# Kernel optimization log

Measured on AMD Instinct MI355X. Metric: run time of the kernel, lower is better.

## Reference

```python
import jax, jax.numpy as jnp
import numpy as np

N_NODES = 100000
IMPROVED_FILL = 2.0  # improved=True in GCNConv -> self-loop weight 2.0


def setup_inputs() -> dict:
    key = jax.random.key(0)
    k1, k2, k3 = jax.random.split(key, 3)
    x = jax.random.normal(k1, (N_NODES, 128), dtype=jnp.float32)
    edge_index = jax.random.randint(k2, (2, 640000), 0, N_NODES, dtype=jnp.int64)
    # Glorot-style init like PyG's GCNConv weight
    W = jax.random.normal(k3, (128, 128), dtype=jnp.float32) * (1.0 / np.sqrt(128))
    b = jnp.zeros((128,), dtype=jnp.float32)
    return {"x": x, "edge_index": edge_index, "W": W, "b": b}


def reference(x, edge_index, W, b):
    N = x.shape[0]
    E = edge_index.shape[1]
    # --- gcn_norm with improved self-loops (fill value 2.0) ---
    loop = jnp.arange(N, dtype=edge_index.dtype)
    row = jnp.concatenate([edge_index[0], loop])  # source nodes
    col = jnp.concatenate([edge_index[1], loop])  # target nodes
    ew = jnp.concatenate([jnp.ones((E,), x.dtype), jnp.full((N,), IMPROVED_FILL, x.dtype)])
    deg = jax.ops.segment_sum(ew, col, num_segments=N)
    dinv = jnp.where(deg > 0, jax.lax.rsqrt(deg), 0.0)
    norm = dinv[row] * ew * dinv[col]  # [E+N]
    # --- linear transform then normalized scatter-add aggregation ---
    xW = x @ W  # [N, out]
    msgs = norm[:, None] * xW[row]  # [E+N, out]
    out = jax.ops.segment_sum(msgs, col, num_segments=N)
    return out + b
```

## Files before the change

kernel.cpp:

```cpp
#include <hip/hip_runtime.h>

#define GCN_N 100000
#define GCN_E 640000
#define GCN_F 128
#define NPB  32
#define CAP  32
#define ZROW 100000

typedef __attribute__((ext_vector_type(8))) short bf16x8;
typedef __attribute__((ext_vector_type(4))) float f32x4;
typedef __attribute__((ext_vector_type(8))) unsigned short ushort8;

__device__ inline unsigned short f2bf(float f) {
    unsigned u = __float_as_uint(f);
    return (unsigned short)((u + 0x7fff + ((u >> 16) & 1)) >> 16);
}
__device__ inline float bflo(unsigned u) { return __uint_as_float(u << 16); }
__device__ inline float bfhi(unsigned u) { return __uint_as_float(u & 0xffff0000u); }

__global__ void fill_ell(const int* __restrict__ rows, const int* __restrict__ cols,
                         int* __restrict__ cnt, int* __restrict__ ell) {
    int i = blockIdx.x * 256 + threadIdx.x;
    int4 r = ((const int4*)rows)[i];
    int4 c = ((const int4*)cols)[i];
    int k;
    k = atomicAdd(&cnt[c.x], 1); if (k < CAP) ell[(size_t)c.x * CAP + k] = r.x;
    k = atomicAdd(&cnt[c.y], 1); if (k < CAP) ell[(size_t)c.y * CAP + k] = r.y;
    k = atomicAdd(&cnt[c.z], 1); if (k < CAP) ell[(size_t)c.z * CAP + k] = r.z;
    k = atomicAdd(&cnt[c.w], 1); if (k < CAP) ell[(size_t)c.w * CAP + k] = r.w;
}

__global__ void scale_conv(const float* __restrict__ x, const int* __restrict__ cnt,
                           ushort* __restrict__ xs, const float* __restrict__ W,
                           ushort* __restrict__ wfh, ushort* __restrict__ wfl) {
    int blk = blockIdx.x;
    int t = threadIdx.x;
    if (blk >= 12501) {
        int p    = blk - 12501;
        int pi   = p * 4 + (t >> 6);
        int lane = t & 63;
        int kt = pi >> 3, nt = pi & 7;
        int kr   = kt * 32 + ((lane >> 4) * 8);
        int ncol = nt * 16 + (lane & 15);
        ushort8 hv, lv;
#pragma unroll
        for (int j = 0; j < 8; ++j) {
            float w = W[(size_t)(kr + j) * GCN_F + ncol];
            unsigned short h = f2bf(w);
            hv[j] = h;
            lv[j] = f2bf(w - bflo((unsigned)h));
        }
        size_t fo = (size_t)(kt * 8 + nt) * 64 + lane;
        ((ushort8*)wfh)[fo] = hv;
        ((ushort8*)wfl)[fo] = lv;
        return;
    }
    if (blk == 12500) {
        if (t < 32) ((ushort4*)xs)[(size_t)ZROW * 32 + t] = make_ushort4(0, 0, 0, 0);
        return;
    }
    int i = blk * 256 + t;
    int node = i >> 5;
    float di = rsqrtf(2.0f + (float)cnt[node]);
    float4 v = ((const float4*)x)[i];
    ushort4 o;
    o.x = f2bf(di * v.x); o.y = f2bf(di * v.y);
    o.z = f2bf(di * v.z); o.w = f2bf(di * v.w);
    ((ushort4*)xs)[i] = o;
}

__global__ __launch_bounds__(256) void gcn_fused(
        const ushort* __restrict__ xs, const int* __restrict__ cnt,
        const int* __restrict__ ell, const ushort* __restrict__ wfh,
        const ushort* __restrict__ wfl, const float* __restrict__ b,
        float* __restrict__ out) {
    __shared__ ushort Ah[NPB * GCN_F];
    __shared__ ushort Al[NPB * GCN_F];
    __shared__ int    sell[NPB * CAP];
    __shared__ int    scnt[NPB];
    int t = threadIdx.x;
    int row0 = blockIdx.x * NPB;

    if (t < NPB) scnt[t] = cnt[row0 + t];
    __syncthreads();

    for (int i = t; i < NPB * CAP; i += 256) {
        int rr = i >> 5, kk = i & (CAP - 1);
        int v = ell[(size_t)(row0 + rr) * CAP + kk];
        int dg = scnt[rr]; if (dg > CAP) dg = CAP;
        sell[i] = (kk < dg) ? v : ZROW;
    }
    __syncthreads();

    int lane = t & 63;
    int wv   = t >> 6;

    {
        const unsigned* xs2 = (const unsigned*)xs;
        for (int q = 0; q < 8; ++q) {
            int rr = wv * 8 + q;
            int c  = row0 + rr;
            int deg = scnt[rr]; if (deg > CAP) deg = CAP;
            const int* sp = &sell[rr * CAP];
            int4 m0 = *(const int4*)sp;
            int4 m1 = *(const int4*)(sp + 4);
            unsigned sv = xs2[c * 64 + lane];
            unsigned v0 = xs2[m0.x * 64 + lane];
            unsigned v1 = xs2[m0.y * 64 + lane];
            unsigned v2 = xs2[m0.z * 64 + lane];
            unsigned v3 = xs2[m0.w * 64 + lane];
            unsigned v4 = xs2[m1.x * 64 + lane];
            unsigned v5 = xs2[m1.y * 64 + lane];
            unsigned v6 = xs2[m1.z * 64 + lane];
            unsigned v7 = xs2[m1.w * 64 + lane];
            float ax = 2.0f * bflo(sv);
            float ay = 2.0f * bfhi(sv);
            ax += bflo(v0) + bflo(v1) + bflo(v2) + bflo(v3)
                + bflo(v4) + bflo(v5) + bflo(v6) + bflo(v7);
            ay += bfhi(v0) + bfhi(v1) + bfhi(v2) + bfhi(v3)
                + bfhi(v4) + bfhi(v5) + bfhi(v6) + bfhi(v7);
            if (deg > 8) {
                for (int k = 8; k < deg; k += 4) {
                    int4 m = *(const int4*)(sp + k);
                    unsigned u0 = xs2[m.x * 64 + lane];
                    unsigned u1 = xs2[m.y * 64 + lane];
                    unsigned u2 = xs2[m.z * 64 + lane];
                    unsigned u3 = xs2[m.w * 64 + lane];
                    ax += bflo(u0) + bflo(u1) + bflo(u2) + bflo(u3);
                    ay += bfhi(u0) + bfhi(u1) + bfhi(u2) + bfhi(u3);
                }
            }
            float di = rsqrtf(2.0f + (float)scnt[rr]);
            float axd = di * ax, ayd = di * ay;
            unsigned short hx = f2bf(axd), hy = f2bf(ayd);
            unsigned short lx = f2bf(axd - bflo((unsigned)hx));
            unsigned short ly = f2bf(ayd - bflo((unsigned)hy));
            unsigned off = (unsigned)rr * 256 + (((unsigned)lane * 4) ^ (((unsigned)(rr & 7)) << 4));
            *(unsigned*)((char*)Ah + off) = ((unsigned)hy << 16) | hx;
            *(unsigned*)((char*)Al + off) = ((unsigned)ly << 16) | lx;
        }
    }
    __syncthreads();

    int lrow  = lane & 15;
    int lhalf = lane >> 4;
    f32x4 acc[2][2];
#pragma unroll
    for (int m = 0; m < 2; ++m)
#pragma unroll
        for (int n = 0; n < 2; ++n) acc[m][n] = (f32x4)0.f;

    const bf16x8* whp = (const bf16x8*)wfh;
    const bf16x8* wlp = (const bf16x8*)wfl;
    int nt0 = wv * 2;

#pragma unroll
    for (int kt = 0; kt < 4; ++kt) {
        unsigned kb = ((unsigned)(kt * 64 + lhalf * 16)) ^ (((unsigned)(lane & 7)) << 4);
        unsigned o0 = (unsigned)lrow * 256 + kb;
        bf16x8 ah[2], al[2], wh[2], wl[2];
        ah[0] = *(const bf16x8*)((const char*)Ah + o0);
        ah[1] = *(const bf16x8*)((const char*)Ah + o0 + 4096);
        al[0] = *(const bf16x8*)((const char*)Al + o0);
        al[1] = *(const bf16x8*)((const char*)Al + o0 + 4096);
        wh[0] = whp[(kt * 8 + nt0) * 64 + lane];
        wh[1] = whp[(kt * 8 + nt0 + 1) * 64 + lane];
        wl[0] = wlp[(kt * 8 + nt0) * 64 + lane];
        wl[1] = wlp[(kt * 8 + nt0 + 1) * 64 + lane];
#pragma unroll
        for (int m = 0; m < 2; ++m)
#pragma unroll
            for (int n = 0; n < 2; ++n) {
                acc[m][n] = __builtin_amdgcn_mfma_f32_16x16x32_bf16(ah[m], wh[n], acc[m][n], 0, 0, 0);
                acc[m][n] = __builtin_amdgcn_mfma_f32_16x16x32_bf16(ah[m], wl[n], acc[m][n], 0, 0, 0);
                acc[m][n] = __builtin_amdgcn_mfma_f32_16x16x32_bf16(al[m], wh[n], acc[m][n], 0, 0, 0);
            }
    }

    float b0 = b[wv * 32 + lrow];
    float b1 = b[wv * 32 + 16 + lrow];
#pragma unroll
    for (int m = 0; m < 2; ++m)
#pragma unroll
        for (int n = 0; n < 2; ++n) {
            int col = wv * 32 + n * 16 + lrow;
            float bb = n ? b1 : b0;
#pragma unroll
            for (int j = 0; j < 4; ++j) {
                int r = row0 + m * 16 + lhalf * 4 + j;
                out[(size_t)r * GCN_F + col] = acc[m][n][j] + bb;
            }
        }
}

extern "C" void kernel_launch(void* const* d_in, const int* in_sizes, int n_in,
                              void* d_out, int out_size, void* d_ws, size_t ws_size,
                              hipStream_t stream) {
    const float* x  = (const float*)d_in[0];
    const int*   ei = (const int*)d_in[1];
    const float* W  = (const float*)d_in[2];
    const float* b  = (const float*)d_in[3];
    float* out = (float*)d_out;

    const int N = GCN_N, E = GCN_E;
    const int* rows = ei;
    const int* cols = ei + E;

    char*   ws  = (char*)d_ws;
    int*    cnt = (int*)(ws + 0);
    int*    ell = (int*)(ws + 400384);
    ushort* xs  = (ushort*)(ws + 13200384);
    ushort* wfh = (ushort*)(ws + 38800640);
    ushort* wfl = (ushort*)(ws + 38833408);

    hipMemsetAsync(cnt, 0, (size_t)N * sizeof(int), stream);
    fill_ell<<<E / 1024, 256, 0, stream>>>(rows, cols, cnt, ell);
    scale_conv<<<12509, 256, 0, stream>>>(x, cnt, xs, W, wfh, wfl);
    gcn_fused<<<N / NPB, 256, 0, stream>>>(xs, cnt, ell, wfh, wfl, b, out);
}
```

Before: 182.9 us.

## Merge all GCN stages into one persistent kernel with grid barriers

Replaces the memset and three separate launches with a single persistent kernel of 1024 blocks that runs zeroing, ELL fill, feature scaling and the fused aggregate+GEMM stage, separated by software grid barriers. The ELL array is now pre-filled with the zero-row index, so the per-tile padding logic goes away and the adjacency tile loads straight into shared memory. Launch overhead and inter-kernel gaps are removed. In exchange it adds a full 12.8MB ELL initialization write, atomic spin barriers, and relies on all 1024 blocks being co-resident. Edge processing also drops from 4 edges per thread with int4 loads to grid-stride scalar loads.

```diff
diff --git a/kernel.cpp b/kernel.cpp
--- a/kernel.cpp
+++ b/kernel.cpp
@@ -6,6 +6,8 @@
 #define NPB  32
 #define CAP  32
 #define ZROW 100000
+#define GRID 1024
+#define TTOT (GRID * 256)
 
 typedef __attribute__((ext_vector_type(8))) short bf16x8;
 typedef __attribute__((ext_vector_type(4))) float f32x4;
@@ -18,89 +20,106 @@
 __device__ inline float bflo(unsigned u) { return __uint_as_float(u << 16); }
 __device__ inline float bfhi(unsigned u) { return __uint_as_float(u & 0xffff0000u); }
 
-__global__ void fill_ell(const int* __restrict__ rows, const int* __restrict__ cols,
-                         int* __restrict__ cnt, int* __restrict__ ell) {
-    int i = blockIdx.x * 256 + threadIdx.x;
-    int4 r = ((const int4*)rows)[i];
-    int4 c = ((const int4*)cols)[i];
-    int k;
-    k = atomicAdd(&cnt[c.x], 1); if (k < CAP) ell[(size_t)c.x * CAP + k] = r.x;
-    k = atomicAdd(&cnt[c.y], 1); if (k < CAP) ell[(size_t)c.y * CAP + k] = r.y;
-    k = atomicAdd(&cnt[c.z], 1); if (k < CAP) ell[(size_t)c.z * CAP + k] = r.z;
-    k = atomicAdd(&cnt[c.w], 1); if (k < CAP) ell[(size_t)c.w * CAP + k] = r.w;
-}
-
-__global__ void scale_conv(const float* __restrict__ x, const int* __restrict__ cnt,
-                           ushort* __restrict__ xs, const float* __restrict__ W,
-                           ushort* __restrict__ wfh, ushort* __restrict__ wfl) {
-    int blk = blockIdx.x;
-    int t = threadIdx.x;
-    if (blk >= 12501) {
-        int p    = blk - 12501;
-        int pi   = p * 4 + (t >> 6);
-        int lane = t & 63;
-        int kt = pi >> 3, nt = pi & 7;
-        int kr   = kt * 32 + ((lane >> 4) * 8);
-        int ncol = nt * 16 + (lane & 15);
-        ushort8 hv, lv;
-#pragma unroll
-        for (int j = 0; j < 8; ++j) {
-            float w = W[(size_t)(kr + j) * GCN_F + ncol];
-            unsigned short h = f2bf(w);
-            hv[j] = h;
-            lv[j] = f2bf(w - bflo((unsigned)h));
-        }
-        size_t fo = (size_t)(kt * 8 + nt) * 64 + lane;
-        ((ushort8*)wfh)[fo] = hv;
-        ((ushort8*)wfl)[fo] = lv;
-        return;
-    }
-    if (blk == 12500) {
-        if (t < 32) ((ushort4*)xs)[(size_t)ZROW * 32 + t] = make_ushort4(0, 0, 0, 0);
-        return;
-    }
-    int i = blk * 256 + t;
-    int node = i >> 5;
-    float di = rsqrtf(2.0f + (float)cnt[node]);
-    float4 v = ((const float4*)x)[i];
-    ushort4 o;
-    o.x = f2bf(di * v.x); o.y = f2bf(di * v.y);
-    o.z = f2bf(di * v.z); o.w = f2bf(di * v.w);
-    ((ushort4*)xs)[i] = o;
-}
-
-__global__ __launch_bounds__(256) void gcn_fused(
-        const ushort* __restrict__ xs, const int* __restrict__ cnt,
-        const int* __restrict__ ell, const ushort* __restrict__ wfh,
-        const ushort* __restrict__ wfl, const float* __restrict__ b,
-        float* __restrict__ out) {
+__device__ inline void grid_barrier(int* bar) {
+    __syncthreads();
+    if (threadIdx.x == 0) {
+        __threadfence();
+        int g = __hip_atomic_load(&bar[1], __ATOMIC_RELAXED, __HIP_MEMORY_SCOPE_AGENT);
+        int a = __hip_atomic_fetch_add(&bar[0], 1, __ATOMIC_ACQ_REL, __HIP_MEMORY_SCOPE_AGENT);
+        if (a == GRID - 1) {
+            __hip_atomic_store(&bar[0], 0, __ATOMIC_RELAXED, __HIP_MEMORY_SCOPE_AGENT);
+            __hip_atomic_fetch_add(&bar[1], 1, __ATOMIC_RELEASE, __HIP_MEMORY_SCOPE_AGENT);
+        } else {
+            while (__hip_atomic_load(&bar[1], __ATOMIC_ACQUIRE, __HIP_MEMORY_SCOPE_AGENT) == g) {
+                __builtin_amdgcn_s_sleep(2);
+            }
+        }
+        __threadfence();
+    }
+    __syncthreads();
+}
+
+__global__ __launch_bounds__(256, 4) void gcn_all(
+        const float* __restrict__ x, const int* __restrict__ rows,
+        const int* __restrict__ cols, const float* __restrict__ W,
+        const float* __restrict__ b, int* __restrict__ cnt,
+        int* __restrict__ ell, ushort* __restrict__ xs,
+        ushort* __restrict__ wfh, ushort* __restrict__ wfl,
+        float* __restrict__ out, int* __restrict__ bar) {
     __shared__ ushort Ah[NPB * GCN_F];
     __shared__ ushort Al[NPB * GCN_F];
     __shared__ int    sell[NPB * CAP];
-    __shared__ int    scnt[NPB];
-    int t = threadIdx.x;
-    int row0 = blockIdx.x * NPB;
-
-    if (t < NPB) scnt[t] = cnt[row0 + t];
-    __syncthreads();
-
-    for (int i = t; i < NPB * CAP; i += 256) {
-        int rr = i >> 5, kk = i & (CAP - 1);
-        int v = ell[(size_t)(row0 + rr) * CAP + kk];
-        int dg = scnt[rr]; if (dg > CAP) dg = CAP;
-        sell[i] = (kk < dg) ? v : ZROW;
-    }
-    __syncthreads();
-
-    int lane = t & 63;
-    int wv   = t >> 6;
+
+    int t   = threadIdx.x;
+    int tid = blockIdx.x * 256 + t;
 
     {
-        const unsigned* xs2 = (const unsigned*)xs;
+        int4 z4 = make_int4(0, 0, 0, 0);
+        for (int i = tid; i < GCN_N / 4; i += TTOT) ((int4*)cnt)[i] = z4;
+        int4 zr = make_int4(ZROW, ZROW, ZROW, ZROW);
+        for (int i = tid; i < GCN_N * CAP / 4; i += TTOT) ((int4*)ell)[i] = zr;
+        if (tid < 32) ((ushort4*)xs)[(size_t)ZROW * 32 + tid] = make_ushort4(0, 0, 0, 0);
+        if (tid >= 2048 && tid < 4096) {
+            int pi   = (tid - 2048) >> 6;
+            int lane = tid & 63;
+            int kt = pi >> 3, nt = pi & 7;
+            int kr   = kt * 32 + ((lane >> 4) * 8);
+            int ncol = nt * 16 + (lane & 15);
+            ushort8 hv, lv;
+#pragma unroll
+            for (int j = 0; j < 8; ++j) {
+                float w = W[(size_t)(kr + j) * GCN_F + ncol];
+                unsigned short h = f2bf(w);
+                hv[j] = h;
+                lv[j] = f2bf(w - bflo((unsigned)h));
+            }
+            size_t fo = (size_t)(kt * 8 + nt) * 64 + lane;
+            ((ushort8*)wfh)[fo] = hv;
+            ((ushort8*)wfl)[fo] = lv;
+        }
+    }
+    grid_barrier(bar);
+
+    for (int e = tid; e < GCN_E; e += TTOT) {
+        int c = cols[e], r = rows[e];
+        int k = atomicAdd(&cnt[c], 1);
+        if (k < CAP) ell[(size_t)c * CAP + k] = r;
+    }
+    grid_barrier(bar);
+
+    for (int i = tid; i < GCN_N * 32; i += TTOT) {
+        int node = i >> 5;
+        float di = rsqrtf(2.0f + (float)cnt[node]);
+        float4 v = ((const float4*)x)[i];
+        ushort4 o;
+        o.x = f2bf(di * v.x); o.y = f2bf(di * v.y);
+        o.z = f2bf(di * v.z); o.w = f2bf(di * v.w);
+        ((ushort4*)xs)[i] = o;
+    }
+    grid_barrier(bar);
+
+    int lane  = t & 63;
+    int wv    = t >> 6;
+    int lrow  = lane & 15;
+    int lhalf = lane >> 4;
+    const unsigned* xs2 = (const unsigned*)xs;
+    const bf16x8* whp = (const bf16x8*)wfh;
+    const bf16x8* wlp = (const bf16x8*)wfl;
+    int nt0 = wv * 2;
+
+    for (int tile = blockIdx.x; tile < GCN_N / NPB; tile += GRID) {
+        int row0 = tile * NPB;
+
+        const int4* esrc = (const int4*)(ell + (size_t)row0 * CAP);
+        ((int4*)sell)[t]       = esrc[t];
+        ((int4*)sell)[t + 256] = esrc[t + 256];
+        __syncthreads();
+
         for (int q = 0; q < 8; ++q) {
             int rr = wv * 8 + q;
             int c  = row0 + rr;
-            int deg = scnt[rr]; if (deg > CAP) deg = CAP;
+            int degc = __builtin_amdgcn_readfirstlane(cnt[c]);
+            int deg  = degc > CAP ? CAP : degc;
             const int* sp = &sell[rr * CAP];
             int4 m0 = *(const int4*)sp;
             int4 m1 = *(const int4*)(sp + 4);
@@ -130,7 +149,7 @@
                     ay += bfhi(u0) + bfhi(u1) + bfhi(u2) + bfhi(u3);
                 }
             }
-            float di = rsqrtf(2.0f + (float)scnt[rr]);
+            float di = rsqrtf(2.0f + (float)degc);
             float axd = di * ax, ayd = di * ay;
             unsigned short hx = f2bf(axd), hy = f2bf(ayd);
             unsigned short lx = f2bf(axd - bflo((unsigned)hx));
@@ -139,58 +158,52 @@
             *(unsigned*)((char*)Ah + off) = ((unsigned)hy << 16) | hx;
             *(unsigned*)((char*)Al + off) = ((unsigned)ly << 16) | lx;
         }
-    }
-    __syncthreads();
-
-    int lrow  = lane & 15;
-    int lhalf = lane >> 4;
-    f32x4 acc[2][2];
-#pragma unroll
-    for (int m = 0; m < 2; ++m)
-#pragma unroll
-        for (int n = 0; n < 2; ++n) acc[m][n] = (f32x4)0.f;
-
-    const bf16x8* whp = (const bf16x8*)wfh;
-    const bf16x8* wlp = (const bf16x8*)wfl;
-    int nt0 = wv * 2;
-
-#pragma unroll
-    for (int kt = 0; kt < 4; ++kt) {
-        unsigned kb = ((unsigned)(kt * 64 + lhalf * 16)) ^ (((unsigned)(lane & 7)) << 4);
-        unsigned o0 = (unsigned)lrow * 256 + kb;
-        bf16x8 ah[2], al[2], wh[2], wl[2];
-        ah[0] = *(const bf16x8*)((const char*)Ah + o0);
-        ah[1] = *(const bf16x8*)((const char*)Ah + o0 + 4096);
-        al[0] = *(const bf16x8*)((const char*)Al + o0);
-        al[1] = *(const bf16x8*)((const char*)Al + o0 + 4096);
-        wh[0] = whp[(kt * 8 + nt0) * 64 + lane];
-        wh[1] = whp[(kt * 8 + nt0 + 1) * 64 + lane];
-        wl[0] = wlp[(kt * 8 + nt0) * 64 + lane];
-        wl[1] = wlp[(kt * 8 + nt0 + 1) * 64 + lane];
+        __syncthreads();
+
+        f32x4 acc[2][2];
 #pragma unroll
         for (int m = 0; m < 2; ++m)
 #pragma unroll
+            for (int n = 0; n < 2; ++n) acc[m][n] = (f32x4)0.f;
+
+#pragma unroll
+        for (int kt = 0; kt < 4; ++kt) {
+            unsigned kb = ((unsigned)(kt * 64 + lhalf * 16)) ^ (((unsigned)(lane & 7)) << 4);
+            unsigned o0 = (unsigned)lrow * 256 + kb;
+            bf16x8 ah[2], al[2], wh[2], wl[2];
+            ah[0] = *(const bf16x8*)((const char*)Ah + o0);
+            ah[1] = *(const bf16x8*)((const char*)Ah + o0 + 4096);
+            al[0] = *(const bf16x8*)((const char*)Al + o0);
+            al[1] = *(const bf16x8*)((const char*)Al + o0 + 4096);
+            wh[0] = whp[(kt * 8 + nt0) * 64 + lane];
+            wh[1] = whp[(kt * 8 + nt0 + 1) * 64 + lane];
+            wl[0] = wlp[(kt * 8 + nt0) * 64 + lane];
+            wl[1] = wlp[(kt * 8 + nt0 + 1) * 64 + lane];
+#pragma unroll
+            for (int m = 0; m < 2; ++m)
+#pragma unroll
+                for (int n = 0; n < 2; ++n) {
+                    acc[m][n] = __builtin_amdgcn_mfma_f32_16x16x32_bf16(ah[m], wh[n], acc[m][n], 0, 0, 0);
+                    acc[m][n] = __builtin_amdgcn_mfma_f32_16x16x32_bf16(ah[m], wl[n], acc[m][n], 0, 0, 0);
+                    acc[m][n] = __builtin_amdgcn_mfma_f32_16x16x32_bf16(al[m], wh[n], acc[m][n], 0, 0, 0);
+                }
+        }
+
+        float b0 = b[wv * 32 + lrow];
+        float b1 = b[wv * 32 + 16 + lrow];
+#pragma unroll
+        for (int m = 0; m < 2; ++m)
+#pragma unroll
             for (int n = 0; n < 2; ++n) {
-                acc[m][n] = __builtin_amdgcn_mfma_f32_16x16x32_bf16(ah[m], wh[n], acc[m][n], 0, 0, 0);
-                acc[m][n] = __builtin_amdgcn_mfma_f32_16x16x32_bf16(ah[m], wl[n], acc[m][n], 0, 0, 0);
-                acc[m][n] = __builtin_amdgcn_mfma_f32_16x16x32_bf16(al[m], wh[n], acc[m][n], 0, 0, 0);
-            }
-    }
-
-    float b0 = b[wv * 32 + lrow];
-    float b1 = b[wv * 32 + 16 + lrow];
-#pragma unroll
-    for (int m = 0; m < 2; ++m)
-#pragma unroll
-        for (int n = 0; n < 2; ++n) {
-            int col = wv * 32 + n * 16 + lrow;
-            float bb = n ? b1 : b0;
-#pragma unroll
-            for (int j = 0; j < 4; ++j) {
-                int r = row0 + m * 16 + lhalf * 4 + j;
-                out[(size_t)r * GCN_F + col] = acc[m][n][j] + bb;
-            }
-        }
+                int col = wv * 32 + n * 16 + lrow;
+                float bb = n ? b1 : b0;
+#pragma unroll
+                for (int j = 0; j < 4; ++j) {
+                    int r = row0 + m * 16 + lhalf * 4 + j;
+                    out[(size_t)r * GCN_F + col] = acc[m][n][j] + bb;
+                }
+            }
+    }
 }
 
 extern "C" void kernel_launch(void* const* d_in, const int* in_sizes, int n_in,
@@ -202,19 +215,17 @@
     const float* b  = (const float*)d_in[3];
     float* out = (float*)d_out;
 
-    const int N = GCN_N, E = GCN_E;
     const int* rows = ei;
-    const int* cols = ei + E;
+    const int* cols = ei + GCN_E;
 
     char*   ws  = (char*)d_ws;
     int*    cnt = (int*)(ws + 0);
+    int*    bar = (int*)(ws + 400000);
     int*    ell = (int*)(ws + 400384);
     ushort* xs  = (ushort*)(ws + 13200384);
     ushort* wfh = (ushort*)(ws + 38800640);
     ushort* wfl = (ushort*)(ws + 38833408);
 
-    hipMemsetAsync(cnt, 0, (size_t)N * sizeof(int), stream);
-    fill_ell<<<E / 1024, 256, 0, stream>>>(rows, cols, cnt, ell);
-    scale_conv<<<12509, 256, 0, stream>>>(x, cnt, xs, W, wfh, wfl);
-    gcn_fused<<<N / NPB, 256, 0, stream>>>(xs, cnt, ell, wfh, wfl, b, out);
-}
+    hipMemsetAsync(bar, 0, 2 * sizeof(int), stream);
+    gcn_all<<<GRID, 256, 0, stream>>>(x, rows, cols, W, b, cnt, ell, xs, wfh, wfl, out, bar);
+}
```

New measurement: 643.8 us. 252% more time.

## Merge ELL build and bf16 conversion into one kernel, apply source degree scaling in gather

Applied to the files above, without the earlier changes.

The ELL fill, the unscaled bf16 conversion of x and the W split are merged into a single launch. x conversion no longer depends on degree counts, so it can run alongside the atomic fill. The per-source rsqrt(deg) scaling moves into the gather loop, which now loads the neighbor's count for every edge. The unrolled gather is widened to 16 neighbors with a scalar tail. This removes one launch and the dependency between stages, at the cost of extra cnt gathers and rsqrt work per edge and more loads issued against padding rows.

```diff
diff --git a/kernel.cpp b/kernel.cpp
--- a/kernel.cpp
+++ b/kernel.cpp
@@ -18,55 +18,50 @@
 __device__ inline float bflo(unsigned u) { return __uint_as_float(u << 16); }
 __device__ inline float bfhi(unsigned u) { return __uint_as_float(u & 0xffff0000u); }
 
-__global__ void fill_ell(const int* __restrict__ rows, const int* __restrict__ cols,
-                         int* __restrict__ cnt, int* __restrict__ ell) {
-    int i = blockIdx.x * 256 + threadIdx.x;
-    int4 r = ((const int4*)rows)[i];
-    int4 c = ((const int4*)cols)[i];
-    int k;
-    k = atomicAdd(&cnt[c.x], 1); if (k < CAP) ell[(size_t)c.x * CAP + k] = r.x;
-    k = atomicAdd(&cnt[c.y], 1); if (k < CAP) ell[(size_t)c.y * CAP + k] = r.y;
-    k = atomicAdd(&cnt[c.z], 1); if (k < CAP) ell[(size_t)c.z * CAP + k] = r.z;
-    k = atomicAdd(&cnt[c.w], 1); if (k < CAP) ell[(size_t)c.w * CAP + k] = r.w;
-}
-
-__global__ void scale_conv(const float* __restrict__ x, const int* __restrict__ cnt,
-                           ushort* __restrict__ xs, const float* __restrict__ W,
-                           ushort* __restrict__ wfh, ushort* __restrict__ wfl) {
+__global__ void fill_xs(const int* __restrict__ rows, const int* __restrict__ cols,
+                        int* __restrict__ cnt, int* __restrict__ ell,
+                        const float* __restrict__ x, ushort* __restrict__ xs,
+                        const float* __restrict__ W,
+                        ushort* __restrict__ wfh, ushort* __restrict__ wfl) {
     int blk = blockIdx.x;
     int t = threadIdx.x;
-    if (blk >= 12501) {
-        int p    = blk - 12501;
-        int pi   = p * 4 + (t >> 6);
-        int lane = t & 63;
-        int kt = pi >> 3, nt = pi & 7;
-        int kr   = kt * 32 + ((lane >> 4) * 8);
-        int ncol = nt * 16 + (lane & 15);
-        ushort8 hv, lv;
-#pragma unroll
-        for (int j = 0; j < 8; ++j) {
-            float w = W[(size_t)(kr + j) * GCN_F + ncol];
-            unsigned short h = f2bf(w);
-            hv[j] = h;
-            lv[j] = f2bf(w - bflo((unsigned)h));
-        }
-        size_t fo = (size_t)(kt * 8 + nt) * 64 + lane;
-        ((ushort8*)wfh)[fo] = hv;
-        ((ushort8*)wfl)[fo] = lv;
+    if (blk < 2500) {
+        int e = blk * 256 + t;
+        int c = cols[e], r = rows[e];
+        int k = atomicAdd(&cnt[c], 1);
+        if (k < CAP) ell[(size_t)c * CAP + k] = r;
         return;
     }
-    if (blk == 12500) {
+    if (blk < 15000) {
+        int i = (blk - 2500) * 256 + t;
+        float4 v = ((const float4*)x)[i];
+        ushort4 o;
+        o.x = f2bf(v.x); o.y = f2bf(v.y);
+        o.z = f2bf(v.z); o.w = f2bf(v.w);
+        ((ushort4*)xs)[i] = o;
+        return;
+    }
+    if (blk == 15000) {
         if (t < 32) ((ushort4*)xs)[(size_t)ZROW * 32 + t] = make_ushort4(0, 0, 0, 0);
         return;
     }
-    int i = blk * 256 + t;
-    int node = i >> 5;
-    float di = rsqrtf(2.0f + (float)cnt[node]);
-    float4 v = ((const float4*)x)[i];
-    ushort4 o;
-    o.x = f2bf(di * v.x); o.y = f2bf(di * v.y);
-    o.z = f2bf(di * v.z); o.w = f2bf(di * v.w);
-    ((ushort4*)xs)[i] = o;
+    int p    = blk - 15001;
+    int pi   = p * 4 + (t >> 6);
+    int lane = t & 63;
+    int kt = pi >> 3, nt = pi & 7;
+    int kr   = kt * 32 + ((lane >> 4) * 8);
+    int ncol = nt * 16 + (lane & 15);
+    ushort8 hv, lv;
+#pragma unroll
+    for (int j = 0; j < 8; ++j) {
+        float w = W[(size_t)(kr + j) * GCN_F + ncol];
+        unsigned short h = f2bf(w);
+        hv[j] = h;
+        lv[j] = f2bf(w - bflo((unsigned)h));
+    }
+    size_t fo = (size_t)(kt * 8 + nt) * 64 + lane;
+    ((ushort8*)wfh)[fo] = hv;
+    ((ushort8*)wfl)[fo] = lv;
 }
 
 __global__ __launch_bounds__(256) void gcn_fused(
@@ -100,38 +95,52 @@
         for (int q = 0; q < 8; ++q) {
             int rr = wv * 8 + q;
             int c  = row0 + rr;
-            int deg = scnt[rr]; if (deg > CAP) deg = CAP;
             const int* sp = &sell[rr * CAP];
             int4 m0 = *(const int4*)sp;
             int4 m1 = *(const int4*)(sp + 4);
-            unsigned sv = xs2[c * 64 + lane];
-            unsigned v0 = xs2[m0.x * 64 + lane];
-            unsigned v1 = xs2[m0.y * 64 + lane];
-            unsigned v2 = xs2[m0.z * 64 + lane];
-            unsigned v3 = xs2[m0.w * 64 + lane];
-            unsigned v4 = xs2[m1.x * 64 + lane];
-            unsigned v5 = xs2[m1.y * 64 + lane];
-            unsigned v6 = xs2[m1.z * 64 + lane];
-            unsigned v7 = xs2[m1.w * 64 + lane];
-            float ax = 2.0f * bflo(sv);
-            float ay = 2.0f * bfhi(sv);
-            ax += bflo(v0) + bflo(v1) + bflo(v2) + bflo(v3)
-                + bflo(v4) + bflo(v5) + bflo(v6) + bflo(v7);
-            ay += bfhi(v0) + bfhi(v1) + bfhi(v2) + bfhi(v3)
-                + bfhi(v4) + bfhi(v5) + bfhi(v6) + bfhi(v7);
-            if (deg > 8) {
-                for (int k = 8; k < deg; k += 4) {
-                    int4 m = *(const int4*)(sp + k);
-                    unsigned u0 = xs2[m.x * 64 + lane];
-                    unsigned u1 = xs2[m.y * 64 + lane];
-                    unsigned u2 = xs2[m.z * 64 + lane];
-                    unsigned u3 = xs2[m.w * 64 + lane];
-                    ax += bflo(u0) + bflo(u1) + bflo(u2) + bflo(u3);
-                    ay += bfhi(u0) + bfhi(u1) + bfhi(u2) + bfhi(u3);
+            int4 m2 = *(const int4*)(sp + 8);
+            int4 m3 = *(const int4*)(sp + 12);
+            unsigned s0 = xs2[c * 64 + lane];
+            unsigned v[16];
+            int cq[16];
+            v[ 0] = xs2[m0.x * 64 + lane]; cq[ 0] = cnt[m0.x];
+            v[ 1] = xs2[m0.y * 64 + lane]; cq[ 1] = cnt[m0.y];
+            v[ 2] = xs2[m0.z * 64 + lane]; cq[ 2] = cnt[m0.z];
+            v[ 3] = xs2[m0.w * 64 + lane]; cq[ 3] = cnt[m0.w];
+            v[ 4] = xs2[m1.x * 64 + lane]; cq[ 4] = cnt[m1.x];
+            v[ 5] = xs2[m1.y * 64 + lane]; cq[ 5] = cnt[m1.y];
+            v[ 6] = xs2[m1.z * 64 + lane]; cq[ 6] = cnt[m1.z];
+            v[ 7] = xs2[m1.w * 64 + lane]; cq[ 7] = cnt[m1.w];
+            v[ 8] = xs2[m2.x * 64 + lane]; cq[ 8] = cnt[m2.x];
+            v[ 9] = xs2[m2.y * 64 + lane]; cq[ 9] = cnt[m2.y];
+            v[10] = xs2[m2.z * 64 + lane]; cq[10] = cnt[m2.z];
+            v[11] = xs2[m2.w * 64 + lane]; cq[11] = cnt[m2.w];
+            v[12] = xs2[m3.x * 64 + lane]; cq[12] = cnt[m3.x];
+            v[13] = xs2[m3.y * 64 + lane]; cq[13] = cnt[m3.y];
+            v[14] = xs2[m3.z * 64 + lane]; cq[14] = cnt[m3.z];
+            v[15] = xs2[m3.w * 64 + lane]; cq[15] = cnt[m3.w];
+            int dc = scnt[rr];
+            float dic = rsqrtf(2.0f + (float)dc);
+            float sw  = 2.0f * dic;
+            float ax = sw * bflo(s0);
+            float ay = sw * bfhi(s0);
+#pragma unroll
+            for (int k = 0; k < 16; ++k) {
+                float dm = rsqrtf(2.0f + (float)cq[k]);
+                ax = fmaf(dm, bflo(v[k]), ax);
+                ay = fmaf(dm, bfhi(v[k]), ay);
+            }
+            int deg = dc > CAP ? CAP : dc;
+            if (deg > 16) {
+                for (int k = 16; k < deg; ++k) {
+                    int m = sp[k];
+                    unsigned u = xs2[m * 64 + lane];
+                    float dm = rsqrtf(2.0f + (float)cnt[m]);
+                    ax = fmaf(dm, bflo(u), ax);
+                    ay = fmaf(dm, bfhi(u), ay);
                 }
             }
-            float di = rsqrtf(2.0f + (float)scnt[rr]);
-            float axd = di * ax, ayd = di * ay;
+            float axd = dic * ax, ayd = dic * ay;
             unsigned short hx = f2bf(axd), hy = f2bf(ayd);
             unsigned short lx = f2bf(axd - bflo((unsigned)hx));
             unsigned short ly = f2bf(ayd - bflo((unsigned)hy));
@@ -213,8 +222,7 @@
     ushort* wfh = (ushort*)(ws + 38800640);
     ushort* wfl = (ushort*)(ws + 38833408);
 
-    hipMemsetAsync(cnt, 0, (size_t)N * sizeof(int), stream);
-    fill_ell<<<E / 1024, 256, 0, stream>>>(rows, cols, cnt, ell);
-    scale_conv<<<12509, 256, 0, stream>>>(x, cnt, xs, W, wfh, wfl);
+    hipMemsetAsync(cnt, 0, (size_t)(N + 1) * sizeof(int), stream);
+    fill_xs<<<15009, 256, 0, stream>>>(rows, cols, cnt, ell, x, xs, W, wfh, wfl);
     gcn_fused<<<N / NPB, 256, 0, stream>>>(xs, cnt, ell, wfh, wfl, b, out);
 }
```

Measured after the change: 194.9 us. 6.6% more time.

## Pre-fill ELL with zero-row sentinel and gather 16 neighbors directly from global

Applied to the files above, without the earlier changes.

A new kernel fills the ELL table with the zero-row index before edges are scattered, so padding slots already point at a zero row. The fused kernel then drops the shared-memory staging of ELL indices and counts and its two barriers, reading indices straight from global memory. It unconditionally gathers 16 neighbor rows per node instead of 8, then handles any remainder one at a time. The edge fill now uses one edge per thread and gcn_fused asks for 8 blocks per CU. The cost is an extra 12.8 MB write pass and more wasted gathers of the zero row for low-degree nodes.

```diff
diff --git a/kernel.cpp b/kernel.cpp
--- a/kernel.cpp
+++ b/kernel.cpp
@@ -18,16 +18,17 @@
 __device__ inline float bflo(unsigned u) { return __uint_as_float(u << 16); }
 __device__ inline float bfhi(unsigned u) { return __uint_as_float(u & 0xffff0000u); }
 
+__global__ void init_ell(int* __restrict__ ell) {
+    int i = blockIdx.x * 256 + threadIdx.x;
+    ((int4*)ell)[i] = make_int4(ZROW, ZROW, ZROW, ZROW);
+}
+
 __global__ void fill_ell(const int* __restrict__ rows, const int* __restrict__ cols,
                          int* __restrict__ cnt, int* __restrict__ ell) {
-    int i = blockIdx.x * 256 + threadIdx.x;
-    int4 r = ((const int4*)rows)[i];
-    int4 c = ((const int4*)cols)[i];
-    int k;
-    k = atomicAdd(&cnt[c.x], 1); if (k < CAP) ell[(size_t)c.x * CAP + k] = r.x;
-    k = atomicAdd(&cnt[c.y], 1); if (k < CAP) ell[(size_t)c.y * CAP + k] = r.y;
-    k = atomicAdd(&cnt[c.z], 1); if (k < CAP) ell[(size_t)c.z * CAP + k] = r.z;
-    k = atomicAdd(&cnt[c.w], 1); if (k < CAP) ell[(size_t)c.w * CAP + k] = r.w;
+    int e = blockIdx.x * 256 + threadIdx.x;
+    int c = cols[e], r = rows[e];
+    int k = atomicAdd(&cnt[c], 1);
+    if (k < CAP) ell[(size_t)c * CAP + k] = r;
 }
 
 __global__ void scale_conv(const float* __restrict__ x, const int* __restrict__ cnt,
@@ -69,29 +70,15 @@
     ((ushort4*)xs)[i] = o;
 }
 
-__global__ __launch_bounds__(256) void gcn_fused(
+__global__ __launch_bounds__(256, 8) void gcn_fused(
         const ushort* __restrict__ xs, const int* __restrict__ cnt,
         const int* __restrict__ ell, const ushort* __restrict__ wfh,
         const ushort* __restrict__ wfl, const float* __restrict__ b,
         float* __restrict__ out) {
     __shared__ ushort Ah[NPB * GCN_F];
     __shared__ ushort Al[NPB * GCN_F];
-    __shared__ int    sell[NPB * CAP];
-    __shared__ int    scnt[NPB];
     int t = threadIdx.x;
     int row0 = blockIdx.x * NPB;
-
-    if (t < NPB) scnt[t] = cnt[row0 + t];
-    __syncthreads();
-
-    for (int i = t; i < NPB * CAP; i += 256) {
-        int rr = i >> 5, kk = i & (CAP - 1);
-        int v = ell[(size_t)(row0 + rr) * CAP + kk];
-        int dg = scnt[rr]; if (dg > CAP) dg = CAP;
-        sell[i] = (kk < dg) ? v : ZROW;
-    }
-    __syncthreads();
-
     int lane = t & 63;
     int wv   = t >> 6;
 
@@ -100,37 +87,43 @@
         for (int q = 0; q < 8; ++q) {
             int rr = wv * 8 + q;
             int c  = row0 + rr;
-            int deg = scnt[rr]; if (deg > CAP) deg = CAP;
-            const int* sp = &sell[rr * CAP];
-            int4 m0 = *(const int4*)sp;
-            int4 m1 = *(const int4*)(sp + 4);
-            unsigned sv = xs2[c * 64 + lane];
-            unsigned v0 = xs2[m0.x * 64 + lane];
-            unsigned v1 = xs2[m0.y * 64 + lane];
-            unsigned v2 = xs2[m0.z * 64 + lane];
-            unsigned v3 = xs2[m0.w * 64 + lane];
-            unsigned v4 = xs2[m1.x * 64 + lane];
-            unsigned v5 = xs2[m1.y * 64 + lane];
-            unsigned v6 = xs2[m1.z * 64 + lane];
-            unsigned v7 = xs2[m1.w * 64 + lane];
-            float ax = 2.0f * bflo(sv);
-            float ay = 2.0f * bfhi(sv);
-            ax += bflo(v0) + bflo(v1) + bflo(v2) + bflo(v3)
-                + bflo(v4) + bflo(v5) + bflo(v6) + bflo(v7);
-            ay += bfhi(v0) + bfhi(v1) + bfhi(v2) + bfhi(v3)
-                + bfhi(v4) + bfhi(v5) + bfhi(v6) + bfhi(v7);
-            if (deg > 8) {
-                for (int k = 8; k < deg; k += 4) {
-                    int4 m = *(const int4*)(sp + k);
-                    unsigned u0 = xs2[m.x * 64 + lane];
-                    unsigned u1 = xs2[m.y * 64 + lane];
-                    unsigned u2 = xs2[m.z * 64 + lane];
-                    unsigned u3 = xs2[m.w * 64 + lane];
-                    ax += bflo(u0) + bflo(u1) + bflo(u2) + bflo(u3);
-                    ay += bfhi(u0) + bfhi(u1) + bfhi(u2) + bfhi(u3);
+            const int4* ep = (const int4*)(ell + (size_t)c * CAP);
+            int4 m0 = ep[0];
+            int4 m1 = ep[1];
+            int4 m2 = ep[2];
+            int4 m3 = ep[3];
+            int dc = cnt[c];
+            unsigned s0 = xs2[c * 64 + lane];
+            unsigned v[16];
+            v[ 0] = xs2[m0.x * 64 + lane];
+            v[ 1] = xs2[m0.y * 64 + lane];
+            v[ 2] = xs2[m0.z * 64 + lane];
+            v[ 3] = xs2[m0.w * 64 + lane];
+            v[ 4] = xs2[m1.x * 64 + lane];
+            v[ 5] = xs2[m1.y * 64 + lane];
+            v[ 6] = xs2[m1.z * 64 + lane];
+            v[ 7] = xs2[m1.w * 64 + lane];
+            v[ 8] = xs2[m2.x * 64 + lane];
+            v[ 9] = xs2[m2.y * 64 + lane];
+            v[10] = xs2[m2.z * 64 + lane];
+            v[11] = xs2[m2.w * 64 + lane];
+            v[12] = xs2[m3.x * 64 + lane];
+            v[13] = xs2[m3.y * 64 + lane];
+            v[14] = xs2[m3.z * 64 + lane];
+            v[15] = xs2[m3.w * 64 + lane];
+            float ax = 2.0f * bflo(s0);
+            float ay = 2.0f * bfhi(s0);
+#pragma unroll
+            for (int k = 0; k < 16; ++k) { ax += bflo(v[k]); ay += bfhi(v[k]); }
+            int deg = dc > CAP ? CAP : dc;
+            if (deg > 16) {
+                for (int k = 16; k < deg; ++k) {
+                    int m = ((const int*)ep)[k];
+                    unsigned u = xs2[m * 64 + lane];
+                    ax += bflo(u); ay += bfhi(u);
                 }
             }
-            float di = rsqrtf(2.0f + (float)scnt[rr]);
+            float di = rsqrtf(2.0f + (float)dc);
             float axd = di * ax, ayd = di * ay;
             unsigned short hx = f2bf(axd), hy = f2bf(ayd);
             unsigned short lx = f2bf(axd - bflo((unsigned)hx));
@@ -214,7 +207,8 @@
     ushort* wfl = (ushort*)(ws + 38833408);
 
     hipMemsetAsync(cnt, 0, (size_t)N * sizeof(int), stream);
-    fill_ell<<<E / 1024, 256, 0, stream>>>(rows, cols, cnt, ell);
+    init_ell<<<3125, 256, 0, stream>>>(ell);
+    fill_ell<<<E / 256, 256, 0, stream>>>(rows, cols, cnt, ell);
     scale_conv<<<12509, 256, 0, stream>>>(x, cnt, xs, W, wfh, wfl);
     gcn_fused<<<N / NPB, 256, 0, stream>>>(xs, cnt, ell, wfh, wfl, b, out);
 }
```

Result: no change. 182.2 us (-0.4%).
